# Kernel optimization log

Measured on AMD Instinct MI355X. Metric: run time of the kernel, lower is better.

Reference implementation:

```python
import jax, jax.numpy as jnp
import numpy as np

EMBED_DIM = 1024
HEADS = 16
HEAD_DIM = EMBED_DIM // HEADS
ROPE_THETA = 10000.0


def apply_rope(x):
    # x: [B, H, T, D]; standard rotary embedding on head_dim, half-split style
    D = x.shape[-1]
    T = x.shape[-2]
    half = D // 2
    inv_freq = 1.0 / (ROPE_THETA ** (jnp.arange(half, dtype=jnp.float32) / half))
    ang = jnp.arange(T, dtype=jnp.float32)[:, None] * inv_freq[None, :]  # [T, half]
    cos, sin = jnp.cos(ang), jnp.sin(ang)  # [T, half]
    x1, x2 = x[..., :half], x[..., half:]
    return jnp.concatenate([x1 * cos - x2 * sin, x1 * sin + x2 * cos], axis=-1)


def setup_inputs() -> dict:
    key = jax.random.key(0)
    ks = jax.random.split(key, 6)
    B, T, E, H = 2, 2048, EMBED_DIM, HEADS
    s = 0.02
    return {
        "x": jax.random.normal(ks[0], (B, T, E), dtype=jnp.float32),
        "w_qkv": jax.random.normal(ks[1], (E, 3 * E), dtype=jnp.float32) * s,
        "w_pre": jax.random.normal(ks[2], (H, H), dtype=jnp.float32) * s,
        "w_post": jax.random.normal(ks[3], (H, H), dtype=jnp.float32) * s,
        "w_out": jax.random.normal(ks[4], (E, E), dtype=jnp.float32) * s,
        "b_out": jax.random.normal(ks[5], (E,), dtype=jnp.float32) * s,
    }


def reference(x, w_qkv, w_pre, w_post, w_out, b_out):
    B, T, E = x.shape
    H, D = HEADS, HEAD_DIM
    qkv = x @ w_qkv  # [B, T, 3E]
    q, k, v = jnp.split(qkv, 3, axis=-1)
    q = q.reshape(B, T, H, D).transpose(0, 2, 1, 3)  # [B,H,T,D]
    k = k.reshape(B, T, H, D).transpose(0, 2, 1, 3)
    v = v.reshape(B, T, H, D).transpose(0, 2, 1, 3)
    q = apply_rope(q)
    k = apply_rope(k)
    scale = D ** -0.5
    dots = jnp.einsum('bhid,bhjd->bhij', q, k) * scale  # [B,H,T,T]
    # pre-softmax talking-heads mixing: new_head g = sum_h w_pre[g,h] * dots[h]
    dots = jnp.einsum('bhij,gh->bgij', dots, w_pre)
    attn = jax.nn.softmax(dots, axis=-1)
    # post-softmax mixing
    attn = jnp.einsum('bhij,gh->bgij', attn, w_post)
    out = jnp.einsum('bhij,bhjd->bhid', attn, v)  # [B,H,T,D]
    out = out.transpose(0, 2, 1, 3).reshape(B, T, E)
    return out @ w_out.T + b_out  # dropout is identity in eval
```

## Files before the change

### kernel.cpp

```cpp
#include <hip/hip_runtime.h>
#include <stdint.h>

typedef unsigned short u16;
typedef unsigned int   u32;

#define T_SEQ 2048
#define NB 2
#define NH 16
#define HD 64
#define E_DIM 1024
#define E3 3072
#define JS1 4
#define JS2 4
#define S2A 36
#define OS2 1040

#if defined(__has_builtin)
#if __has_builtin(__builtin_amdgcn_mfma_f32_16x16x16f16)
#define MIX16 1
#endif
#endif

#ifdef MIX16
#define S2D 18
#else
#define S2D 36
#endif

typedef float f32x4 __attribute__((ext_vector_type(4)));
typedef short s16x8 __attribute__((ext_vector_type(8)));
#ifdef MIX16
typedef _Float16 f16x4 __attribute__((ext_vector_type(4)));
#endif

__device__ __forceinline__ float b2f(u16 u) {
    union { float f; u32 i; } v; v.i = ((u32)u) << 16; return v.f;
}
__device__ __forceinline__ u16 f2b(float f) {
    union { float f; u32 i; } v; v.f = f;
    u32 x = v.i;
    return (u16)((x + 0x7FFFu + ((x >> 16) & 1u)) >> 16);
}
__device__ __forceinline__ f32x4 mfma_bf16(s16x8 a, s16x8 b, f32x4 c) {
    return __builtin_amdgcn_mfma_f32_16x16x32_bf16(a, b, c, 0, 0, 0);
}
#ifdef MIX16
__device__ __forceinline__ f32x4 mfma_f16_16(f16x4 a, f16x4 b, f32x4 c) {
    return __builtin_amdgcn_mfma_f32_16x16x16f16(a, b, c, 0, 0, 0);
}
#endif
__device__ __forceinline__ void gl_lds16(const void* g, void* l) {
    __builtin_amdgcn_global_load_lds((const __attribute__((address_space(1))) void*)g,
                                     (__attribute__((address_space(3))) void*)l, 16, 0, 0);
}

__global__ void k_detect(const u16* __restrict__ x, int* __restrict__ flag) {
    __shared__ int cnt[256];
    int tid = threadIdx.x;
    int insane = 0;
    for (int i = tid; i < 4096; i += 256) {
        u16 v = x[2 * i];
        int e = (v >> 7) & 0xFF;
        if (e >= 143 || (e > 0 && e <= 100)) insane++;
    }
    cnt[tid] = insane;
    __syncthreads();
    if (tid == 0) {
        int s = 0;
        for (int k = 0; k < 256; ++k) s += cnt[k];
        *flag = (s > 512) ? 1 : 0;
    }
}

__global__ void k_cvt_bf16(const void* __restrict__ src, u16* __restrict__ dst,
                           int n, const int* __restrict__ flag) {
    int i = blockIdx.x * 256 + threadIdx.x;
    bool f32 = (*flag) != 0;
    if (i < n) dst[i] = f32 ? f2b(((const float*)src)[i]) : ((const u16*)src)[i];
}

__global__ void k_cvt_small(const void* __restrict__ a, const void* __restrict__ b,
                            const void* __restrict__ c, float* __restrict__ da,
                            float* __restrict__ db, float* __restrict__ dc,
                            const int* __restrict__ flag) {
    int i = blockIdx.x * 256 + threadIdx.x;
    bool f32 = (*flag) != 0;
    if (i < 256) {
        da[i] = f32 ? ((const float*)a)[i] : b2f(((const u16*)a)[i]);
    } else if (i < 512) {
        int j = i - 256;
        db[j] = f32 ? ((const float*)b)[j] : b2f(((const u16*)b)[j]);
    } else if (i < 1536) {
        int j = i - 512;
        dc[j] = f32 ? ((const float*)c)[j] : b2f(((const u16*)c)[j]);
    }
}

__global__ void k_transpose(const void* __restrict__ w, u16* __restrict__ wT,
                            const int* __restrict__ flag) {
    __shared__ u16 tile[32][33];
    bool f32 = (*flag) != 0;
    int n0 = blockIdx.x * 32;
    int k0 = blockIdx.y * 32;
    int tid = threadIdx.x;
    int c = tid & 31, r4 = tid >> 5;
#pragma unroll
    for (int it = 0; it < 4; ++it) {
        int r = r4 + it * 8;
        size_t idx = (size_t)(k0 + r) * E3 + n0 + c;
        tile[r][c] = f32 ? f2b(((const float*)w)[idx]) : ((const u16*)w)[idx];
    }
    __syncthreads();
#pragma unroll
    for (int it = 0; it < 4; ++it) {
        int r = r4 + it * 8;
        wT[(size_t)(n0 + r) * E_DIM + k0 + c] = tile[c][r];
    }
}

__global__ void k_qkv(const u16* __restrict__ A, const u16* __restrict__ Bm,
                      u16* __restrict__ C) {
    __shared__ __align__(16) u16 As[128 * 32];
    __shared__ __align__(16) u16 Bs[128 * 32];
    int m0 = blockIdx.x * 128, n0 = blockIdx.y * 128;
    int tid = threadIdx.x, lane = tid & 63, wv = tid >> 6;
    int q = lane >> 4, l = lane & 15;
    int wm = (wv >> 1) * 64, wn = (wv & 1) * 64;
    f32x4 acc[4][4] = {};
    int r16 = lane >> 2;
    int ccol = (lane & 3) * 8;
    for (int kc = 0; kc < 1024; kc += 32) {
#pragma unroll
        for (int j = 0; j < 4; ++j) {
            int chunk = wv * 4 + j;
            if (chunk < 8) {
                const u16* g = A + (size_t)(m0 + chunk * 16 + r16) * 1024 + kc + ccol;
                gl_lds16(g, (char*)As + chunk * 1024);
            } else {
                int ch = chunk - 8;
                const u16* g = Bm + (size_t)(n0 + ch * 16 + r16) * 1024 + kc + ccol;
                gl_lds16(g, (char*)Bs + ch * 1024);
            }
        }
        __syncthreads();
        s16x8 af[4], bf[4];
#pragma unroll
        for (int t = 0; t < 4; ++t) {
            af[t] = *(const s16x8*)(As + (wm + t * 16 + l) * 32 + q * 8);
            bf[t] = *(const s16x8*)(Bs + (wn + t * 16 + l) * 32 + q * 8);
        }
#pragma unroll
        for (int i = 0; i < 4; ++i)
#pragma unroll
            for (int j2 = 0; j2 < 4; ++j2)
                acc[i][j2] = mfma_bf16(af[i], bf[j2], acc[i][j2]);
        __syncthreads();
    }
#pragma unroll
    for (int i = 0; i < 4; ++i)
#pragma unroll
        for (int j2 = 0; j2 < 4; ++j2)
#pragma unroll
            for (int r = 0; r < 4; ++r) {
                int row = m0 + wm + i * 16 + q * 4 + r;
                int col = n0 + wn + j2 * 16 + l;
                C[(size_t)row * E3 + col] = f2b(acc[i][j2][r]);
            }
}

__global__ void k_rope(const u16* __restrict__ qkv, u16* __restrict__ qr,
                       u16* __restrict__ kr, u16* __restrict__ vt) {
    __shared__ u16 tile[64][66];
    int t0 = blockIdx.x * 64;
    int h = blockIdx.y, b = blockIdx.z;
    int tid = threadIdx.x;
    const float LN_TH = 9.210340371976184f / 32.0f;
    for (int src = 0; src < 3; ++src) {
        {
            int d = tid & 63, tr = tid >> 6;
#pragma unroll
            for (int it = 0; it < 16; ++it) {
                int t = tr + it * 4;
                tile[t][d] = qkv[(size_t)(b * T_SEQ + t0 + t) * E3 + src * E_DIM + h * HD + d];
            }
        }
        __syncthreads();
        if (src < 2) {
            u16* dst = (src == 0 ? qr : kr) + ((size_t)(b * NH + h) * T_SEQ) * HD;
            int d = tid & 31, tr = tid >> 5;
            float inv = __expf(-(float)d * LN_TH);
#pragma unroll
            for (int it = 0; it < 8; ++it) {
                int t = tr + it * 8;
                float ang = (float)(t0 + t) * inv;
                float sn, cs;
                __sincosf(ang, &sn, &cs);
                float x1 = b2f(tile[t][d]);
                float x2 = b2f(tile[t][d + 32]);
                dst[(size_t)(t0 + t) * HD + d]      = f2b(x1 * cs - x2 * sn);
                dst[(size_t)(t0 + t) * HD + d + 32] = f2b(x1 * sn + x2 * cs);
            }
        } else {
            int tl = tid & 63, dr = tid >> 6;
#pragma unroll
            for (int it = 0; it < 16; ++it) {
                int d = dr + it * 4;
                vt[((size_t)(b * NH + h) * HD + d) * T_SEQ + t0 + tl] = tile[tl][d];
            }
        }
        __syncthreads();
    }
}

__global__ __launch_bounds__(256, 3) void k_pass1(const u16* __restrict__ qr, const u16* __restrict__ kr,
                                                  const float* __restrict__ w_pre, float* __restrict__ lpart) {
    __shared__ __align__(16) u16 dotsb[2 * 256 * S2D];
    int lin = blockIdx.x;
    int combo = lin & 7;
    int b = combo >> 2, js = combo & 3;
    int i0 = (lin >> 3) * 32;
    int tid = threadIdx.x, lane = tid & 63, wv = tid >> 6;
    int q = lane >> 4, l = lane & 15;
#ifndef MIX16
    {
        uint2 z = {0u, 0u};
        uint2* p0 = (uint2*)(dotsb + tid * S2D + 16);
        uint2* p1 = (uint2*)(dotsb + 256 * S2D + tid * S2D + 16);
        p0[0] = z; p0[1] = z; p0[2] = z; p0[3] = z;
        p1[0] = z; p1[1] = z; p1[2] = z; p1[3] = z;
    }
#endif
#ifdef MIX16
    f16x4 wpre4;
#pragma unroll
    for (int jj = 0; jj < 4; ++jj)
        wpre4[jj] = (_Float16)(w_pre[l * 16 + q * 4 + jj] * 0.125f);
#else
    s16x8 wpre;
#pragma unroll
    for (int jj = 0; jj < 8; ++jj) {
        int hh = q * 8 + jj;
        wpre[jj] = (hh < 16) ? (short)f2b(w_pre[l * 16 + hh] * 0.125f) : (short)0;
    }
#endif
    s16x8 qf[2][4][2];
#pragma unroll
    for (int it = 0; it < 2; ++it)
#pragma unroll
        for (int hl = 0; hl < 4; ++hl) {
            int h = wv * 4 + hl;
            const u16* ptr = qr + ((size_t)(b * NH + h) * T_SEQ + i0 + it * 16 + l) * HD + q * 8;
            qf[it][hl][0] = *(const s16x8*)(ptr);
            qf[it][hl][1] = *(const s16x8*)(ptr + 32);
        }
    float lacc[2][4][4] = {};
    __syncthreads();
    int jbase = js * (T_SEQ / JS1);
    for (int jstep = 0; jstep < (T_SEQ / JS1) / 16; ++jstep) {
        int jh = jbase + jstep * 16;
        s16x8 kf[4][2];
#pragma unroll
        for (int hl = 0; hl < 4; ++hl) {
            int h = wv * 4 + hl;
            const u16* ptr = kr + ((size_t)(b * NH + h) * T_SEQ + jh + l) * HD + q * 8;
            kf[hl][0] = *(const s16x8*)(ptr);
            kf[hl][1] = *(const s16x8*)(ptr + 32);
        }
#pragma unroll
        for (int it = 0; it < 2; ++it) {
            u16* dots = dotsb + (it & 1) * 256 * S2D;
            f32x4 dacc[4];
#pragma unroll
            for (int hl = 0; hl < 4; ++hl) {
                f32x4 z = {};
                z = mfma_bf16(qf[it][hl][0], kf[hl][0], z);
                z = mfma_bf16(qf[it][hl][1], kf[hl][1], z);
                dacc[hl] = z;
            }
#pragma unroll
            for (int r = 0; r < 4; ++r) {
                int row = (q * 4 + r) * 16 + l;
#ifdef MIX16
                union { u32 u[2]; _Float16 h[4]; } pk;
                pk.h[0] = (_Float16)dacc[0][r]; pk.h[1] = (_Float16)dacc[1][r];
                pk.h[2] = (_Float16)dacc[2][r]; pk.h[3] = (_Float16)dacc[3][r];
                u32* dw = (u32*)dots;
                int wi = row * 9 + wv * 2;
                dw[wi] = pk.u[0]; dw[wi + 1] = pk.u[1];
#else
                uint2 pk;
                pk.x = (u32)f2b(dacc[0][r]) | ((u32)f2b(dacc[1][r]) << 16);
                pk.y = (u32)f2b(dacc[2][r]) | ((u32)f2b(dacc[3][r]) << 16);
                *(uint2*)(dots + row * S2D + wv * 4) = pk;
#endif
            }
            __syncthreads();
#pragma unroll
            for (int cl = 0; cl < 4; ++cl) {
                int c = wv * 4 + cl;
                f32x4 s = {};
#ifdef MIX16
                const u32* dr_ = (const u32*)dots;
                int ri = (c * 16 + l) * 9 + q * 2;
                union { u32 u[2]; f16x4 v; } b4;
                b4.u[0] = dr_[ri]; b4.u[1] = dr_[ri + 1];
                s = mfma_f16_16(wpre4, b4.v, s);
#else
                int rbase = (c * 16 + l) * S2D;
                union { uint2 u2[2]; s16x8 v; } bf_;
                bf_.u2[0] = *(const uint2*)(dots + rbase + q * 8);
                bf_.u2[1] = *(const uint2*)(dots + rbase + q * 8 + 4);
                s = mfma_bf16(wpre, bf_.v, s);
#endif
#pragma unroll
                for (int r = 0; r < 4; ++r)
                    lacc[it][cl][r] += __expf(fminf(s[r], 60.0f));
            }
        }
    }
#pragma unroll
    for (int it = 0; it < 2; ++it)
#pragma unroll
        for (int cl = 0; cl < 4; ++cl)
#pragma unroll
            for (int r = 0; r < 4; ++r) {
                float pv = lacc[it][cl][r];
                pv += __shfl_xor(pv, 1);
                pv += __shfl_xor(pv, 2);
                pv += __shfl_xor(pv, 4);
                pv += __shfl_xor(pv, 8);
                if (l == 0) {
                    int g = q * 4 + r;
                    int irow = wv * 4 + cl;
                    lpart[((size_t)(combo * NH + g)) * T_SEQ + i0 + it * 16 + irow] = pv;
                }
            }
}

__global__ __launch_bounds__(256, 2) void k_pass2(const u16* __restrict__ qr, const u16* __restrict__ kr,
                                                  const u16* __restrict__ vt, const float* __restrict__ lpart,
                                                  const float* __restrict__ w_pre, const float* __restrict__ w_post,
                                                  u16* __restrict__ opart) {
    __shared__ __align__(16) u16 smem[256 * S2D + 2 * 256 * S2A];
    __shared__ float linv[2][16][16];
    u16* dots = smem;
    u16* aTb  = smem + 256 * S2D;
    int lin = blockIdx.x;
    int combo = lin & 7;
    int b = combo >> 2, js = combo & 3;
    int i0 = (lin >> 3) * 32;
    int tid = threadIdx.x, lane = tid & 63, wv = tid >> 6;
    int q = lane >> 4, l = lane & 15;
#ifndef MIX16
    {
        uint2 z = {0u, 0u};
        uint2* p0 = (uint2*)(dots + tid * S2D + 16);
        p0[0] = z; p0[1] = z; p0[2] = z; p0[3] = z;
    }
#endif
    {
        int g = tid >> 4, il = tid & 15;
        float s0 = 0.f, s1 = 0.f;
#pragma unroll
        for (int j4 = 0; j4 < 4; ++j4) {
            const float* lp = lpart + ((size_t)((b * 4 + j4) * NH + g)) * T_SEQ + i0;
            s0 += lp[il];
            s1 += lp[16 + il];
        }
        linv[0][g][il] = 1.0f / s0;
        linv[1][g][il] = 1.0f / s1;
    }
#ifdef MIX16
    f16x4 wpre4, wpost4;
#pragma unroll
    for (int jj = 0; jj < 4; ++jj) {
        wpre4[jj]  = (_Float16)(w_pre[l * 16 + q * 4 + jj] * 0.125f);
        wpost4[jj] = (_Float16)(w_post[l * 16 + q * 4 + jj]);
    }
#else
    s16x8 wpre, wpost;
#pragma unroll
    for (int jj = 0; jj < 8; ++jj) {
        int hh = q * 8 + jj;
        wpre[jj]  = (hh < 16) ? (short)f2b(w_pre[l * 16 + hh] * 0.125f) : (short)0;
        wpost[jj] = (hh < 16) ? (short)f2b(w_post[l * 16 + hh]) : (short)0;
    }
#endif
    s16x8 qf[2][4][2];
#pragma unroll
    for (int it = 0; it < 2; ++it)
#pragma unroll
        for (int hl = 0; hl < 4; ++hl) {
            int h = wv * 4 + hl;
            const u16* ptr = qr + ((size_t)(b * NH + h) * T_SEQ + i0 + it * 16 + l) * HD + q * 8;
            qf[it][hl][0] = *(const s16x8*)(ptr);
            qf[it][hl][1] = *(const s16x8*)(ptr + 32);
        }
    f32x4 oacc[2][4][4] = {};
    __syncthreads();
    int jbase = js * (T_SEQ / JS2);
    for (int jst = 0; jst < (T_SEQ / JS2) / 32; ++jst) {
        int j0 = jbase + jst * 32;
#pragma unroll
        for (int jb = 0; jb < 2; ++jb) {
            int jh = j0 + jb * 16;
            s16x8 kf[4][2];
#pragma unroll
            for (int hl = 0; hl < 4; ++hl) {
                int h = wv * 4 + hl;
                const u16* ptr = kr + ((size_t)(b * NH + h) * T_SEQ + jh + l) * HD + q * 8;
                kf[hl][0] = *(const s16x8*)(ptr);
                kf[hl][1] = *(const s16x8*)(ptr + 32);
            }
#pragma unroll
            for (int it = 0; it < 2; ++it) {
                f32x4 dacc[4];
#pragma unroll
                for (int hl = 0; hl < 4; ++hl) {
                    f32x4 z = {};
                    z = mfma_bf16(qf[it][hl][0], kf[hl][0], z);
                    z = mfma_bf16(qf[it][hl][1], kf[hl][1], z);
                    dacc[hl] = z;
                }
#pragma unroll
                for (int r = 0; r < 4; ++r) {
                    int row = (q * 4 + r) * 16 + l;
#ifdef MIX16
                    union { u32 u[2]; _Float16 h[4]; } pk;
                    pk.h[0] = (_Float16)dacc[0][r]; pk.h[1] = (_Float16)dacc[1][r];
                    pk.h[2] = (_Float16)dacc[2][r]; pk.h[3] = (_Float16)dacc[3][r];
                    u32* dw = (u32*)dots;
                    int wi = row * 9 + wv * 2;
                    dw[wi] = pk.u[0]; dw[wi + 1] = pk.u[1];
#else
                    uint2 pk;
                    pk.x = (u32)f2b(dacc[0][r]) | ((u32)f2b(dacc[1][r]) << 16);
                    pk.y = (u32)f2b(dacc[2][r]) | ((u32)f2b(dacc[3][r]) << 16);
                    *(uint2*)(dots + row * S2D + wv * 4) = pk;
#endif
                }
                __syncthreads();
                u16* aT = aTb + it * 256 * S2A;
#pragma unroll
                for (int cl = 0; cl < 4; ++cl) {
                    int c = wv * 4 + cl;
                    f32x4 s = {};
#ifdef MIX16
                    const u32* dr_ = (const u32*)dots;
                    int ri = (c * 16 + l) * 9 + q * 2;
                    union { u32 u[2]; f16x4 v; } b4;
                    b4.u[0] = dr_[ri]; b4.u[1] = dr_[ri + 1];
                    s = mfma_f16_16(wpre4, b4.v, s);
                    f16x4 pf;
#pragma unroll
                    for (int r = 0; r < 4; ++r)
                        pf[r] = (_Float16)(__expf(fminf(s[r], 60.0f)) * linv[it][q * 4 + r][c]);
                    f32x4 a = {};
                    a = mfma_f16_16(wpost4, pf, a);
#else
                    int rbase = (c * 16 + l) * S2D;
                    union { uint2 u2[2]; s16x8 v; } bf_;
                    bf_.u2[0] = *(const uint2*)(dots + rbase + q * 8);
                    bf_.u2[1] = *(const uint2*)(dots + rbase + q * 8 + 4);
                    s = mfma_bf16(wpre, bf_.v, s);
                    u32 pkx, pky;
                    {
                        u16 pu[4];
#pragma unroll
                        for (int r = 0; r < 4; ++r)
                            pu[r] = f2b(__expf(fminf(s[r], 60.0f)) * linv[it][q * 4 + r][c]);
                        pkx = (u32)pu[0] | ((u32)pu[1] << 16);
                        pky = (u32)pu[2] | ((u32)pu[3] << 16);
                    }
                    int srcA = (q & 1) * 32 + l;
                    int srcB = srcA + 16;
                    u32 x0 = (u32)__shfl((int)pkx, srcA);
                    u32 x1 = (u32)__shfl((int)pky, srcA);
                    u32 x2 = (u32)__shfl((int)pkx, srcB);
                    u32 x3 = (u32)__shfl((int)pky, srcB);
                    union { u32 u[4]; s16x8 v; } pf_;
                    bool hi = (q >= 2);
                    pf_.u[0] = hi ? 0u : x0;
                    pf_.u[1] = hi ? 0u : x1;
                    pf_.u[2] = hi ? 0u : x2;
                    pf_.u[3] = hi ? 0u : x3;
                    f32x4 a = {};
                    a = mfma_bf16(wpost, pf_.v, a);
#endif
#pragma unroll
                    for (int r = 0; r < 4; ++r)
                        aT[((q * 4 + r) * 16 + c) * S2A + jb * 16 + l] = f2b(a[r]);
                }
                __syncthreads();
            }
        }
#pragma unroll
        for (int gl = 0; gl < 4; ++gl) {
            int gp = wv * 4 + gl;
            int ar = (gp * 16 + l) * S2A;
            union { uint2 u2[2]; s16x8 v; } af0, af1;
            af0.u2[0] = *(const uint2*)(aTb + ar + q * 8);
            af0.u2[1] = *(const uint2*)(aTb + ar + q * 8 + 4);
            af1.u2[0] = *(const uint2*)(aTb + 256 * S2A + ar + q * 8);
            af1.u2[1] = *(const uint2*)(aTb + 256 * S2A + ar + q * 8 + 4);
            const u16* vp = vt + ((size_t)(b * NH + gp) * HD) * T_SEQ + j0 + q * 8;
#pragma unroll
            for (int dt = 0; dt < 4; ++dt) {
                s16x8 bfrag = *(const s16x8*)(vp + (size_t)(dt * 16 + l) * T_SEQ);
                oacc[0][gl][dt] = mfma_bf16(af0.v, bfrag, oacc[0][gl][dt]);
                oacc[1][gl][dt] = mfma_bf16(af1.v, bfrag, oacc[1][gl][dt]);
            }
        }
    }
    size_t obase = (size_t)js * ((size_t)NB * T_SEQ * E_DIM);
#pragma unroll
    for (int it = 0; it < 2; ++it) {
        __syncthreads();
        u16* ostage = smem;
#pragma unroll
        for (int gl = 0; gl < 4; ++gl) {
            int gp = wv * 4 + gl;
#pragma unroll
            for (int dt = 0; dt < 4; ++dt)
#pragma unroll
                for (int r = 0; r < 4; ++r)
                    ostage[(q * 4 + r) * OS2 + gp * 64 + dt * 16 + l] = f2b(oacc[it][gl][dt][r]);
        }
        __syncthreads();
        int row = tid >> 4, sl = tid & 15;
        u16* gbase = opart + obase + ((size_t)(b * T_SEQ) + i0 + it * 16 + row) * E_DIM;
#pragma unroll
        for (int w = 0; w < 8; ++w) {
            uint4 v = *(const uint4*)(ostage + row * OS2 + w * 128 + sl * 8);
            *(uint4*)(gbase + w * 128 + sl * 8) = v;
        }
    }
}

__global__ void k_sum(const u16* __restrict__ op, u16* __restrict__ ab) {
    int i = (blockIdx.x * 256 + threadIdx.x) * 8;
    const size_t SZ = (size_t)4096 * 1024;
    union { uint4 v; u16 h[8]; } a0, a1, a2, a3, r;
    a0.v = *(const uint4*)(op + i);
    a1.v = *(const uint4*)(op + SZ + i);
    a2.v = *(const uint4*)(op + 2 * SZ + i);
    a3.v = *(const uint4*)(op + 3 * SZ + i);
#pragma unroll
    for (int k = 0; k < 8; ++k)
        r.h[k] = f2b(b2f(a0.h[k]) + b2f(a1.h[k]) + b2f(a2.h[k]) + b2f(a3.h[k]));
    *(uint4*)(ab + i) = r.v;
}

__global__ void k_outproj(const u16* __restrict__ A, const u16* __restrict__ Bm,
                          const float* __restrict__ bias, void* __restrict__ outv,
                          const int* __restrict__ flag) {
    __shared__ __align__(16) u16 As[128 * 32];
    __shared__ __align__(16) u16 Bs[128 * 32];
    bool f32 = (*flag) != 0;
    int m0 = blockIdx.x * 128, n0 = blockIdx.y * 128;
    int tid = threadIdx.x, lane = tid & 63, wv = tid >> 6;
    int q = lane >> 4, l = lane & 15;
    int wm = (wv >> 1) * 64, wn = (wv & 1) * 64;
    f32x4 acc[4][4] = {};
    int r16 = lane >> 2;
    int ccol = (lane & 3) * 8;
    for (int kc = 0; kc < 1024; kc += 32) {
#pragma unroll
        for (int j = 0; j < 4; ++j) {
            int chunk = wv * 4 + j;
            if (chunk < 8) {
                const u16* g = A + (size_t)(m0 + chunk * 16 + r16) * 1024 + kc + ccol;
                gl_lds16(g, (char*)As + chunk * 1024);
            } else {
                int ch = chunk - 8;
                const u16* g = Bm + (size_t)(n0 + ch * 16 + r16) * 1024 + kc + ccol;
                gl_lds16(g, (char*)Bs + ch * 1024);
            }
        }
        __syncthreads();
        s16x8 af[4], bf[4];
#pragma unroll
        for (int t = 0; t < 4; ++t) {
            af[t] = *(const s16x8*)(As + (wm + t * 16 + l) * 32 + q * 8);
            bf[t] = *(const s16x8*)(Bs + (wn + t * 16 + l) * 32 + q * 8);
        }
#pragma unroll
        for (int i = 0; i < 4; ++i)
#pragma unroll
            for (int j2 = 0; j2 < 4; ++j2)
                acc[i][j2] = mfma_bf16(af[i], bf[j2], acc[i][j2]);
        __syncthreads();
    }
#pragma unroll
    for (int i = 0; i < 4; ++i)
#pragma unroll
        for (int j2 = 0; j2 < 4; ++j2)
#pragma unroll
            for (int r = 0; r < 4; ++r) {
                int row = m0 + wm + i * 16 + q * 4 + r;
                int col = n0 + wn + j2 * 16 + l;
                float val = acc[i][j2][r] + bias[col];
                size_t idx = (size_t)row * E_DIM + col;
                if (f32) ((float*)outv)[idx] = val;
                else     ((u16*)outv)[idx]   = f2b(val);
            }
}

extern "C" void kernel_launch(void* const* d_in, const int* in_sizes, int n_in,
                              void* d_out, int out_size, void* d_ws, size_t ws_size,
                              hipStream_t stream) {
    (void)in_sizes; (void)n_in; (void)out_size; (void)ws_size;
    const void* x      = d_in[0];
    const void* w_qkv  = d_in[1];
    const void* w_pre  = d_in[2];
    const void* w_post = d_in[3];
    const void* w_out  = d_in[4];
    const void* b_out  = d_in[5];

    char* ws = (char*)d_ws;
    size_t off = 0;
    auto alloc = [&](size_t bytes) -> char* {
        char* p = ws + off;
        off += (bytes + 255) & ~(size_t)255;
        return p;
    };
    char* region0 = alloc((size_t)(8 + 6 + 24) * 1024 * 1024);
    u16*  xb      = (u16*)region0;
    u16*  wqkvT   = (u16*)(region0 + (size_t)8 * 1024 * 1024);
    u16*  qkv     = (u16*)(region0 + (size_t)14 * 1024 * 1024);
    u16*  opart   = (u16*)region0;
    int*  flag    = (int*)alloc(256);
    u16*  woutb   = (u16*)alloc((size_t)1024 * 1024 * 2);
    float* wpre_c = (float*)alloc(256 * 4);
    float* wpost_c= (float*)alloc(256 * 4);
    float* bout_c = (float*)alloc(1024 * 4);
    u16*  qr      = (u16*)alloc((size_t)NB * NH * T_SEQ * HD * 2);
    u16*  kr      = (u16*)alloc((size_t)NB * NH * T_SEQ * HD * 2);
    u16*  vt      = (u16*)alloc((size_t)NB * NH * HD * T_SEQ * 2);
    float* lpart  = (float*)alloc((size_t)8 * NH * T_SEQ * 4);
    u16*  ab      = (u16*)alloc((size_t)4096 * 1024 * 2);

    k_detect<<<1, 256, 0, stream>>>((const u16*)x, flag);
    k_cvt_bf16<<<16384, 256, 0, stream>>>(x, xb, 4096 * 1024, flag);
    k_cvt_bf16<<<4096, 256, 0, stream>>>(w_out, woutb, 1024 * 1024, flag);
    k_cvt_small<<<6, 256, 0, stream>>>(w_pre, w_post, b_out, wpre_c, wpost_c, bout_c, flag);
    k_transpose<<<dim3(96, 32), 256, 0, stream>>>(w_qkv, wqkvT, flag);
    k_qkv<<<dim3(32, 24), 256, 0, stream>>>(xb, wqkvT, qkv);
    k_rope<<<dim3(32, 16, 2), 256, 0, stream>>>(qkv, qr, kr, vt);
    k_pass1<<<512, 256, 0, stream>>>(qr, kr, wpre_c, lpart);
    k_pass2<<<512, 256, 0, stream>>>(qr, kr, vt, lpart, wpre_c, wpost_c, opart);
    k_sum<<<2048, 256, 0, stream>>>(opart, ab);
    k_outproj<<<dim3(32, 8), 256, 0, stream>>>(ab, woutb, bout_c, d_out, flag);
}
```

Baseline: 472.4 us.

## Batch both row tiles per barrier in attention passes and fuse partial-sum into out-proj

The pass1 and pass2 attention kernels now write the dots for both 16-row tiles into LDS before a single barrier, which halves the number of __syncthreads per j-step. pass1 also double-buffers across j-steps so consecutive iterations do not overwrite a buffer still being read. The separate k_sum kernel is removed. k_outproj now reads the four partial outputs directly, sums them in registers and stores the result into LDS, which removes one launch and the write and re-read of the intermediate buffer. The cost is more LDS per block, which may lower occupancy, and out-proj A-tile loads that are now synchronous and four times larger instead of async global-to-LDS copies, each reread by all 8 column blocks.

Result: slower. 565.0 us (+19.6%).

```diff
diff --git a/kernel.cpp b/kernel.cpp
--- a/kernel.cpp
+++ b/kernel.cpp
@@ -214,7 +214,7 @@
 
 __global__ __launch_bounds__(256, 3) void k_pass1(const u16* __restrict__ qr, const u16* __restrict__ kr,
                                                   const float* __restrict__ w_pre, float* __restrict__ lpart) {
-    __shared__ __align__(16) u16 dotsb[2 * 256 * S2D];
+    __shared__ __align__(16) u16 dotsb[2 * 2 * 256 * S2D];
     int lin = blockIdx.x;
     int combo = lin & 7;
     int b = combo >> 2, js = combo & 3;
@@ -224,10 +224,11 @@
 #ifndef MIX16
     {
         uint2 z = {0u, 0u};
-        uint2* p0 = (uint2*)(dotsb + tid * S2D + 16);
-        uint2* p1 = (uint2*)(dotsb + 256 * S2D + tid * S2D + 16);
-        p0[0] = z; p0[1] = z; p0[2] = z; p0[3] = z;
-        p1[0] = z; p1[1] = z; p1[2] = z; p1[3] = z;
+#pragma unroll
+        for (int rr = 0; rr < 4; ++rr) {
+            uint2* p0 = (uint2*)(dotsb + (rr * 256 + tid) * S2D + 16);
+            p0[0] = z; p0[1] = z; p0[2] = z; p0[3] = z;
+        }
     }
 #endif
 #ifdef MIX16
@@ -258,6 +259,7 @@
     int jbase = js * (T_SEQ / JS1);
     for (int jstep = 0; jstep < (T_SEQ / JS1) / 16; ++jstep) {
         int jh = jbase + jstep * 16;
+        u16* dots = dotsb + (jstep & 1) * (2 * 256 * S2D);
         s16x8 kf[4][2];
 #pragma unroll
         for (int hl = 0; hl < 4; ++hl) {
@@ -268,7 +270,6 @@
         }
 #pragma unroll
         for (int it = 0; it < 2; ++it) {
-            u16* dots = dotsb + (it & 1) * 256 * S2D;
             f32x4 dacc[4];
 #pragma unroll
             for (int hl = 0; hl < 4; ++hl) {
@@ -279,7 +280,7 @@
             }
 #pragma unroll
             for (int r = 0; r < 4; ++r) {
-                int row = (q * 4 + r) * 16 + l;
+                int row = it * 256 + (q * 4 + r) * 16 + l;
 #ifdef MIX16
                 union { u32 u[2]; _Float16 h[4]; } pk;
                 pk.h[0] = (_Float16)dacc[0][r]; pk.h[1] = (_Float16)dacc[1][r];
@@ -294,19 +295,22 @@
                 *(uint2*)(dots + row * S2D + wv * 4) = pk;
 #endif
             }
-            __syncthreads();
+        }
+        __syncthreads();
+#pragma unroll
+        for (int it = 0; it < 2; ++it)
 #pragma unroll
             for (int cl = 0; cl < 4; ++cl) {
                 int c = wv * 4 + cl;
                 f32x4 s = {};
 #ifdef MIX16
                 const u32* dr_ = (const u32*)dots;
-                int ri = (c * 16 + l) * 9 + q * 2;
+                int ri = (it * 256 + c * 16 + l) * 9 + q * 2;
                 union { u32 u[2]; f16x4 v; } b4;
                 b4.u[0] = dr_[ri]; b4.u[1] = dr_[ri + 1];
                 s = mfma_f16_16(wpre4, b4.v, s);
 #else
-                int rbase = (c * 16 + l) * S2D;
+                int rbase = (it * 256 + c * 16 + l) * S2D;
                 union { uint2 u2[2]; s16x8 v; } bf_;
                 bf_.u2[0] = *(const uint2*)(dots + rbase + q * 8);
                 bf_.u2[1] = *(const uint2*)(dots + rbase + q * 8 + 4);
@@ -316,7 +320,6 @@
                 for (int r = 0; r < 4; ++r)
                     lacc[it][cl][r] += __expf(fminf(s[r], 60.0f));
             }
-        }
     }
 #pragma unroll
     for (int it = 0; it < 2; ++it)
@@ -341,10 +344,10 @@
                                                   const u16* __restrict__ vt, const float* __restrict__ lpart,
                                                   const float* __restrict__ w_pre, const float* __restrict__ w_post,
                                                   u16* __restrict__ opart) {
-    __shared__ __align__(16) u16 smem[256 * S2D + 2 * 256 * S2A];
+    __shared__ __align__(16) u16 smem[2 * 256 * S2D + 2 * 256 * S2A];
     __shared__ float linv[2][16][16];
     u16* dots = smem;
-    u16* aTb  = smem + 256 * S2D;
+    u16* aTb  = smem + 2 * 256 * S2D;
     int lin = blockIdx.x;
     int combo = lin & 7;
     int b = combo >> 2, js = combo & 3;
@@ -354,8 +357,11 @@
 #ifndef MIX16
     {
         uint2 z = {0u, 0u};
-        uint2* p0 = (uint2*)(dots + tid * S2D + 16);
-        p0[0] = z; p0[1] = z; p0[2] = z; p0[3] = z;
+#pragma unroll
+        for (int rr = 0; rr < 2; ++rr) {
+            uint2* p0 = (uint2*)(dots + (rr * 256 + tid) * S2D + 16);
+            p0[0] = z; p0[1] = z; p0[2] = z; p0[3] = z;
+        }
     }
 #endif
     {
@@ -424,7 +430,7 @@
                 }
 #pragma unroll
                 for (int r = 0; r < 4; ++r) {
-                    int row = (q * 4 + r) * 16 + l;
+                    int row = it * 256 + (q * 4 + r) * 16 + l;
 #ifdef MIX16
                     union { u32 u[2]; _Float16 h[4]; } pk;
                     pk.h[0] = (_Float16)dacc[0][r]; pk.h[1] = (_Float16)dacc[1][r];
@@ -439,7 +445,10 @@
                     *(uint2*)(dots + row * S2D + wv * 4) = pk;
 #endif
                 }
-                __syncthreads();
+            }
+            __syncthreads();
+#pragma unroll
+            for (int it = 0; it < 2; ++it) {
                 u16* aT = aTb + it * 256 * S2A;
 #pragma unroll
                 for (int cl = 0; cl < 4; ++cl) {
@@ -447,7 +456,7 @@
                     f32x4 s = {};
 #ifdef MIX16
                     const u32* dr_ = (const u32*)dots;
-                    int ri = (c * 16 + l) * 9 + q * 2;
+                    int ri = (it * 256 + c * 16 + l) * 9 + q * 2;
                     union { u32 u[2]; f16x4 v; } b4;
                     b4.u[0] = dr_[ri]; b4.u[1] = dr_[ri + 1];
                     s = mfma_f16_16(wpre4, b4.v, s);
@@ -458,7 +467,7 @@
                     f32x4 a = {};
                     a = mfma_f16_16(wpost4, pf, a);
 #else
-                    int rbase = (c * 16 + l) * S2D;
+                    int rbase = (it * 256 + c * 16 + l) * S2D;
                     union { uint2 u2[2]; s16x8 v; } bf_;
                     bf_.u2[0] = *(const uint2*)(dots + rbase + q * 8);
                     bf_.u2[1] = *(const uint2*)(dots + rbase + q * 8 + 4);
@@ -491,8 +500,8 @@
                     for (int r = 0; r < 4; ++r)
                         aT[((q * 4 + r) * 16 + c) * S2A + jb * 16 + l] = f2b(a[r]);
                 }
-                __syncthreads();
-            }
+            }
+            __syncthreads();
         }
 #pragma unroll
         for (int gl = 0; gl < 4; ++gl) {
@@ -537,26 +546,13 @@
     }
 }
 
-__global__ void k_sum(const u16* __restrict__ op, u16* __restrict__ ab) {
-    int i = (blockIdx.x * 256 + threadIdx.x) * 8;
-    const size_t SZ = (size_t)4096 * 1024;
-    union { uint4 v; u16 h[8]; } a0, a1, a2, a3, r;
-    a0.v = *(const uint4*)(op + i);
-    a1.v = *(const uint4*)(op + SZ + i);
-    a2.v = *(const uint4*)(op + 2 * SZ + i);
-    a3.v = *(const uint4*)(op + 3 * SZ + i);
-#pragma unroll
-    for (int k = 0; k < 8; ++k)
-        r.h[k] = f2b(b2f(a0.h[k]) + b2f(a1.h[k]) + b2f(a2.h[k]) + b2f(a3.h[k]));
-    *(uint4*)(ab + i) = r.v;
-}
-
-__global__ void k_outproj(const u16* __restrict__ A, const u16* __restrict__ Bm,
+__global__ void k_outproj(const u16* __restrict__ op, const u16* __restrict__ Bm,
                           const float* __restrict__ bias, void* __restrict__ outv,
                           const int* __restrict__ flag) {
     __shared__ __align__(16) u16 As[128 * 32];
     __shared__ __align__(16) u16 Bs[128 * 32];
     bool f32 = (*flag) != 0;
+    const size_t SZ = (size_t)4096 * 1024;
     int m0 = blockIdx.x * 128, n0 = blockIdx.y * 128;
     int tid = threadIdx.x, lane = tid & 63, wv = tid >> 6;
     int q = lane >> 4, l = lane & 15;
@@ -569,8 +565,16 @@
         for (int j = 0; j < 4; ++j) {
             int chunk = wv * 4 + j;
             if (chunk < 8) {
-                const u16* g = A + (size_t)(m0 + chunk * 16 + r16) * 1024 + kc + ccol;
-                gl_lds16(g, (char*)As + chunk * 1024);
+                size_t base = (size_t)(m0 + chunk * 16 + r16) * 1024 + kc + ccol;
+                union { uint4 v; u16 h[8]; } a0, a1, a2, a3, rr;
+                a0.v = *(const uint4*)(op + base);
+                a1.v = *(const uint4*)(op + SZ + base);
+                a2.v = *(const uint4*)(op + 2 * SZ + base);
+                a3.v = *(const uint4*)(op + 3 * SZ + base);
+#pragma unroll
+                for (int k = 0; k < 8; ++k)
+                    rr.h[k] = f2b(b2f(a0.h[k]) + b2f(a1.h[k]) + b2f(a2.h[k]) + b2f(a3.h[k]));
+                *(uint4*)(As + chunk * 512 + r16 * 32 + ccol) = rr.v;
             } else {
                 int ch = chunk - 8;
                 const u16* g = Bm + (size_t)(n0 + ch * 16 + r16) * 1024 + kc + ccol;
@@ -638,7 +642,6 @@
     u16*  kr      = (u16*)alloc((size_t)NB * NH * T_SEQ * HD * 2);
     u16*  vt      = (u16*)alloc((size_t)NB * NH * HD * T_SEQ * 2);
     float* lpart  = (float*)alloc((size_t)8 * NH * T_SEQ * 4);
-    u16*  ab      = (u16*)alloc((size_t)4096 * 1024 * 2);
 
     k_detect<<<1, 256, 0, stream>>>((const u16*)x, flag);
     k_cvt_bf16<<<16384, 256, 0, stream>>>(x, xb, 4096 * 1024, flag);
@@ -649,6 +652,5 @@
     k_rope<<<dim3(32, 16, 2), 256, 0, stream>>>(qkv, qr, kr, vt);
     k_pass1<<<512, 256, 0, stream>>>(qr, kr, wpre_c, lpart);
     k_pass2<<<512, 256, 0, stream>>>(qr, kr, vt, lpart, wpre_c, wpost_c, opart);
-    k_sum<<<2048, 256, 0, stream>>>(opart, ab);
-    k_outproj<<<dim3(32, 8), 256, 0, stream>>>(ab, woutb, bout_c, d_out, flag);
-}
+    k_outproj<<<dim3(32, 8), 256, 0, stream>>>(opart, woutb, bout_c, d_out, flag);
+}
```
